# Performance work log

Measured on AMD Instinct MI355X. Metric: run time of the kernel, lower is better.

Reference implementation:

```python
import jax, jax.numpy as jnp
import numpy as np

B, DV, W, H = 64, 2048, 14, 14
DQ, DA, G, DH, NC = 2400, 1200, 2, 1200, 3000


def setup_inputs() -> dict:
    key = jax.random.key(0)
    ks = jax.random.split(key, 14)
    s = lambda k, shp, scale=0.02: jax.random.normal(k, shp, dtype=jnp.float32) * scale
    return {
        "input_q": jax.random.normal(ks[0], (B, DQ), dtype=jnp.float32),
        "input_v": jax.random.normal(ks[1], (B, DV, W, H), dtype=jnp.float32),
        "Wv_att": s(ks[2], (DA, DV)),
        "bv_att": s(ks[3], (DA,)),
        "Wq_att": s(ks[4], (DA, DQ)),
        "bq_att": s(ks[5], (DA,)),
        "Watt": s(ks[6], (G, DA)),
        "batt": s(ks[7], (G,)),
        "Wv_fus": s(ks[8], (G, DH, DV)),
        "bv_fus": s(ks[9], (G, DH)),
        "Wq_fus": s(ks[10], (G * DH, DQ)),
        "bq_fus": s(ks[11], (G * DH,)),
        "Wc": s(ks[12], (NC, G * DH)),
        "bc": s(ks[13], (NC,)),
    }


def reference(input_q, input_v, Wv_att, bv_att, Wq_att, bq_att, Watt, batt,
              Wv_fus, bv_fus, Wq_fus, bq_fus, Wc, bc):
    b, dv, w, h = input_v.shape
    n = w * h  # spatial positions

    # --- attention branch (eval mode: dropout = identity) ---
    # 1x1 conv == per-position linear over channels; activation_v = tanh
    xv = jnp.tanh(jnp.einsum('bchw,dc->bdhw', input_v, Wv_att) + bv_att[None, :, None, None])
    xv = xv.reshape(b, -1, n).transpose(0, 2, 1)               # [B, WH, DA]
    # question projection; activation_q = tanh
    xq = jnp.tanh(input_q @ Wq_att.T + bq_att)                 # [B, DA]
    # MLB Hadamard fusion + activation_mm = tanh
    xatt = jnp.tanh(xv * xq[:, None, :])                       # [B, WH, DA]
    # glimpse scores: 1x1 conv over dim_mm channels
    wgt = jnp.einsum('bnd,gd->bgn', xatt, Watt) + batt[None, :, None]  # [B, G, WH]
    att = jax.nn.softmax(wgt, axis=-1)                         # softmax over WH per glimpse

    # weighted sum of ORIGINAL features per glimpse
    v_flat = input_v.reshape(b, dv, n)                         # [B, DV, WH]
    v_att = jnp.einsum('bgn,bdn->bgd', att, v_flat)            # [B, G, DV]

    # --- glimpse fusion + classification ---
    v_fus = jnp.tanh(jnp.einsum('bgd,ghd->bgh', v_att, Wv_fus) + bv_fus)  # [B, G, DH]
    v_fus = v_fus.reshape(b, -1)                               # [B, G*DH] (concat over glimpses)
    q_fus = jnp.tanh(input_q @ Wq_fus.T + bq_fus)              # [B, G*DH]
    x = (v_fus * q_fus) @ Wc.T + bc                            # [B, NC]
    return (x, wgt)
```

## Files before the change

### kernel.cpp

```cpp
#include <hip/hip_runtime.h>
#include <hip/hip_fp16.h>

typedef _Float16 half8 __attribute__((ext_vector_type(8)));
typedef float f32x4 __attribute__((ext_vector_type(4)));

__device__ __forceinline__ float tanh_fast(float x) {
  float e = __expf(2.0f * x);
  return 1.0f - 2.0f / (e + 1.0f);
}

__device__ __forceinline__ void gload16(const _Float16* g, _Float16* l) {
  __builtin_amdgcn_global_load_lds((const __attribute__((address_space(1))) void*)g,
                                   (__attribute__((address_space(3))) void*)l,
                                   16, 0, 0);
}

__global__ __launch_bounds__(256) void k_transpose_v(const float* __restrict__ in,
                                                     _Float16* __restrict__ out) {
  __shared__ float t[64][65];
  int b = blockIdx.z;
  int c0 = blockIdx.y * 64;
  int p0 = blockIdx.x * 64;
  int tid = threadIdx.x;
  int pl = tid & 63;
  #pragma unroll
  for (int s = 0; s < 16; ++s) {
    int cl = (tid >> 6) + s * 4;
    int p = p0 + pl;
    t[cl][pl] = (p < 196) ? in[((size_t)b * 2048 + (c0 + cl)) * 196 + p] : 0.0f;
  }
  __syncthreads();
  int c8 = (tid & 7) * 8;
  #pragma unroll
  for (int s = 0; s < 2; ++s) {
    int p = p0 + (tid >> 3) + s * 32;
    if (p < 196) {
      half8 v;
      #pragma unroll
      for (int j = 0; j < 8; ++j) v[j] = (_Float16)t[c8 + j][(tid >> 3) + s * 32];
      *(half8*)(out + ((size_t)b * 196 + p) * 2048 + c0 + c8) = v;
    }
  }
}

__global__ __launch_bounds__(256) void k_prep(const float* __restrict__ W,
                                              _Float16* __restrict__ Wh,
                                              const float* __restrict__ batt,
                                              float* __restrict__ wgt) {
  int i = blockIdx.x * 256 + threadIdx.x;
  int n = i >> 11;
  Wh[i] = (n < 1200) ? (_Float16)W[i] : (_Float16)0.0f;
  if (i < 25088) wgt[i] = batt[(i / 196) & 1];
}

__global__ __launch_bounds__(256) void k_gemm1(const _Float16* __restrict__ A,
                                               const _Float16* __restrict__ B,
                                               const float* __restrict__ bias,
                                               const float* __restrict__ xq,
                                               const float* __restrict__ Watt,
                                               float* __restrict__ wgt) {
  __shared__ __align__(16) _Float16 As[128 * 64];
  __shared__ __align__(16) _Float16 Bs[128 * 64];
  int tid = threadIdx.x;
  int n0 = blockIdx.x * 128;
  int m0 = blockIdx.y * 128;
  int lane = tid & 63;
  int wave = tid >> 6;
  int wm = (wave >> 1) * 64;
  int wn = (wave & 1) * 64;
  int fr = lane & 15;
  int fq = lane >> 4;

  int rsub = lane >> 3;
  int gchunk = (lane & 7) ^ rsub;
  const _Float16* aSrc = A + (size_t)(m0 + wave * 8 + rsub) * 2048 + gchunk * 8;
  const _Float16* bSrc = B + (size_t)(n0 + wave * 8 + rsub) * 2048 + gchunk * 8;
  _Float16* aDst = As + (wave * 8) * 64;
  _Float16* bDst = Bs + (wave * 8) * 64;

  f32x4 acc[4][4];
  #pragma unroll
  for (int i = 0; i < 4; ++i)
    #pragma unroll
    for (int j = 0; j < 4; ++j) acc[i][j] = (f32x4){0.f, 0.f, 0.f, 0.f};

  for (int kt = 0; kt < 32; ++kt) {
    int k0 = kt * 64;
    __syncthreads();
    #pragma unroll
    for (int j = 0; j < 4; ++j) {
      gload16(aSrc + k0 + (size_t)j * 32 * 2048, aDst + j * 32 * 64);
      gload16(bSrc + k0 + (size_t)j * 32 * 2048, bDst + j * 32 * 64);
    }
    __syncthreads();
    #pragma unroll
    for (int s = 0; s < 2; ++s) {
      half8 af[4], bf[4];
      #pragma unroll
      for (int mt = 0; mt < 4; ++mt) {
        int row = wm + mt * 16 + fr;
        af[mt] = *(const half8*)(As + row * 64 + (((s * 4 + fq) ^ (fr & 7)) << 3));
      }
      #pragma unroll
      for (int nt = 0; nt < 4; ++nt) {
        int row = wn + nt * 16 + fr;
        bf[nt] = *(const half8*)(Bs + row * 64 + (((s * 4 + fq) ^ (fr & 7)) << 3));
      }
      #pragma unroll
      for (int mt = 0; mt < 4; ++mt)
        #pragma unroll
        for (int nt = 0; nt < 4; ++nt)
          acc[mt][nt] = __builtin_amdgcn_mfma_f32_16x16x32_f16(af[mt], bf[nt], acc[mt][nt], 0, 0, 0);
    }
  }

  float s0[16], s1[16];
  #pragma unroll
  for (int i = 0; i < 16; ++i) { s0[i] = 0.f; s1[i] = 0.f; }

  #pragma unroll
  for (int nt = 0; nt < 4; ++nt) {
    int col = n0 + wn + nt * 16 + fr;
    bool ok = col < 1200;
    float bcol = ok ? bias[col] : 0.f;
    float wa0 = ok ? Watt[col] : 0.f;
    float wa1 = ok ? Watt[1200 + col] : 0.f;
    #pragma unroll
    for (int mt = 0; mt < 4; ++mt) {
      #pragma unroll
      for (int r = 0; r < 4; ++r) {
        int row = m0 + wm + mt * 16 + fq * 4 + r;
        int b = row / 196;
        float xqv = ok ? xq[b * 1200 + col] : 0.f;
        float xv = tanh_fast(acc[mt][nt][r] + bcol);
        float xa = tanh_fast(xv * xqv);
        s0[mt * 4 + r] += xa * wa0;
        s1[mt * 4 + r] += xa * wa1;
      }
    }
  }
  #pragma unroll
  for (int i = 0; i < 16; ++i) {
    #pragma unroll
    for (int off = 8; off > 0; off >>= 1) {
      s0[i] += __shfl_down(s0[i], off);
      s1[i] += __shfl_down(s1[i], off);
    }
  }
  if (fr == 0) {
    #pragma unroll
    for (int i = 0; i < 16; ++i) {
      int row = m0 + wm + (i >> 2) * 16 + fq * 4 + (i & 3);
      int b = row / 196;
      int p = row - b * 196;
      atomicAdd(&wgt[(b * 2 + 0) * 196 + p], s0[i]);
      atomicAdd(&wgt[(b * 2 + 1) * 196 + p], s1[i]);
    }
  }
}

__global__ __launch_bounds__(64) void k_softmax(const float* __restrict__ wgt,
                                                float* __restrict__ att) {
  int bg = blockIdx.x;
  int lane = threadIdx.x;
  const float* wr = wgt + (size_t)bg * 196;
  float v[4];
  #pragma unroll
  for (int i = 0; i < 4; ++i) {
    int n = lane + i * 64;
    v[i] = (n < 196) ? wr[n] : -1e30f;
  }
  float mx = fmaxf(fmaxf(v[0], v[1]), fmaxf(v[2], v[3]));
  #pragma unroll
  for (int off = 32; off > 0; off >>= 1) mx = fmaxf(mx, __shfl_xor(mx, off));
  float s = 0.f;
  #pragma unroll
  for (int i = 0; i < 4; ++i) {
    int n = lane + i * 64;
    float e = (n < 196) ? __expf(v[i] - mx) : 0.f;
    v[i] = e;
    s += e;
  }
  #pragma unroll
  for (int off = 32; off > 0; off >>= 1) s += __shfl_xor(s, off);
  float inv = 1.f / s;
  #pragma unroll
  for (int i = 0; i < 4; ++i) {
    int n = lane + i * 64;
    if (n < 196) att[(size_t)bg * 196 + n] = v[i] * inv;
  }
}

__global__ __launch_bounds__(256) void k_vatt(const _Float16* __restrict__ Vt,
                                              const float* __restrict__ att,
                                              float* __restrict__ v_att) {
  __shared__ float a0s[196], a1s[196];
  int b = blockIdx.y;
  int tid = threadIdx.x;
  if (tid < 196) {
    a0s[tid] = att[((size_t)b * 2 + 0) * 196 + tid];
    a1s[tid] = att[((size_t)b * 2 + 1) * 196 + tid];
  }
  __syncthreads();
  int d = blockIdx.x * 256 + tid;
  const _Float16* vp = Vt + (size_t)b * 196 * 2048 + d;
  float s0 = 0.f, s1 = 0.f;
  for (int n = 0; n < 196; ++n) {
    float v = (float)vp[(size_t)n * 2048];
    s0 += a0s[n] * v;
    s1 += a1s[n] * v;
  }
  v_att[((size_t)b * 2 + 0) * 2048 + d] = s0;
  v_att[((size_t)b * 2 + 1) * 2048 + d] = s1;
}

__global__ __launch_bounds__(256) void k_skinny(const float* __restrict__ A1,
                                                const float* __restrict__ A2,
                                                int lda, int strideAz,
                                                const float* __restrict__ W, long strideWz,
                                                int N, int K, int S,
                                                float* __restrict__ P, int ldp, int colOffZ) {
  __shared__ __align__(16) float As[32][64];
  __shared__ __align__(16) float Ws2[32][64];
  int tid = threadIdx.x;
  int z = blockIdx.z;
  int s = blockIdx.y;
  int nt0 = blockIdx.x * 64;
  int tiles = K >> 5;
  int t0 = (s * tiles) / S;
  int t1 = ((s + 1) * tiles) / S;
  int tx = tid & 15, ty = tid >> 4;
  int lm = tid >> 2;
  int lk = (tid & 3) * 8;
  const float* Ab = A1 + (size_t)z * strideAz + (size_t)lm * lda;
  const float* A2b = A2 ? (A2 + (size_t)z * strideAz + (size_t)lm * lda) : nullptr;
  int ng = nt0 + lm;
  const float* Wb = W + (size_t)z * strideWz + (size_t)ng * K;
  bool wok = ng < N;
  float acc[4][4] = {};
  for (int t = t0; t < t1; ++t) {
    int k0 = t * 32;
    __syncthreads();
    #pragma unroll
    for (int j = 0; j < 8; ++j) {
      float v = Ab[k0 + lk + j];
      if (A2b) v *= A2b[k0 + lk + j];
      As[lk + j][lm] = v;
    }
    #pragma unroll
    for (int j = 0; j < 8; ++j) Ws2[lk + j][lm] = wok ? Wb[k0 + lk + j] : 0.0f;
    __syncthreads();
    #pragma unroll
    for (int kk = 0; kk < 32; ++kk) {
      f32x4 a = *(const f32x4*)&As[kk][ty * 4];
      f32x4 wv = *(const f32x4*)&Ws2[kk][tx * 4];
      #pragma unroll
      for (int i = 0; i < 4; ++i)
        #pragma unroll
        for (int j = 0; j < 4; ++j) acc[i][j] += a[i] * wv[j];
    }
  }
  #pragma unroll
  for (int i = 0; i < 4; ++i) {
    int m = ty * 4 + i;
    #pragma unroll
    for (int j = 0; j < 4; ++j) {
      int nl = nt0 + tx * 4 + j;
      if (nl < N) P[((size_t)s * 64 + m) * ldp + z * colOffZ + nl] = acc[i][j];
    }
  }
}

__global__ __launch_bounds__(256) void k_combine(const float* __restrict__ P, int S, int ldp,
                                                 const float* __restrict__ bias,
                                                 float* __restrict__ out, int total, int act) {
  int i = blockIdx.x * 256 + threadIdx.x;
  if (i >= total) return;
  int col = i % ldp;
  float sum = bias[col];
  for (int ss = 0; ss < S; ++ss) sum += P[(size_t)ss * total + i];
  out[i] = act ? tanh_fast(sum) : sum;
}

extern "C" void kernel_launch(void* const* d_in, const int* in_sizes, int n_in,
                              void* d_out, int out_size, void* d_ws, size_t ws_size,
                              hipStream_t stream) {
  const float* input_q = (const float*)d_in[0];
  const float* input_v = (const float*)d_in[1];
  const float* Wv_att  = (const float*)d_in[2];
  const float* bv_att  = (const float*)d_in[3];
  const float* Wq_att  = (const float*)d_in[4];
  const float* bq_att  = (const float*)d_in[5];
  const float* Watt    = (const float*)d_in[6];
  const float* batt    = (const float*)d_in[7];
  const float* Wv_fus  = (const float*)d_in[8];
  const float* bv_fus  = (const float*)d_in[9];
  const float* Wq_fus  = (const float*)d_in[10];
  const float* bq_fus  = (const float*)d_in[11];
  const float* Wc      = (const float*)d_in[12];
  const float* bc      = (const float*)d_in[13];
  float* out = (float*)d_out;

  char* ws = (char*)d_ws;
  _Float16* Vt   = (_Float16*)ws; ws += 51380224;
  _Float16* Wh   = (_Float16*)ws; ws += 5242880;
  float* xq      = (float*)ws;    ws += 307200;
  float* att     = (float*)ws;    ws += 100352;
  float* v_att   = (float*)ws;    ws += 1048576;
  float* v_fus   = (float*)ws;    ws += 614400;
  float* q_fus   = (float*)ws;    ws += 614400;
  float* P       = (float*)ws;    ws += 14745600;

  float* x_out   = out;
  float* wgt_out = out + 192000;

  const int S = 16;

  k_transpose_v<<<dim3(4, 32, 64), dim3(256), 0, stream>>>(input_v, Vt);
  k_prep<<<dim3(10240), dim3(256), 0, stream>>>(Wv_att, Wh, batt, wgt_out);

  k_skinny<<<dim3(19, S, 1), dim3(256), 0, stream>>>(input_q, nullptr, 2400, 0,
                                                     Wq_att, 0, 1200, 2400, S, P, 1200, 0);
  k_combine<<<dim3(300), dim3(256), 0, stream>>>(P, S, 1200, bq_att, xq, 76800, 1);

  k_skinny<<<dim3(38, S, 1), dim3(256), 0, stream>>>(input_q, nullptr, 2400, 0,
                                                     Wq_fus, 0, 2400, 2400, S, P + 1228800, 2400, 0);
  k_combine<<<dim3(600), dim3(256), 0, stream>>>(P + 1228800, S, 2400, bq_fus, q_fus, 153600, 1);

  k_gemm1<<<dim3(10, 98), dim3(256), 0, stream>>>(Vt, Wh, bv_att, xq, Watt, wgt_out);

  k_softmax<<<dim3(128), dim3(64), 0, stream>>>(wgt_out, att);

  k_vatt<<<dim3(8, 64), dim3(256), 0, stream>>>(Vt, att, v_att);

  k_skinny<<<dim3(19, S, 2), dim3(256), 0, stream>>>(v_att, nullptr, 4096, 2048,
                                                     Wv_fus, 1200L * 2048L, 1200, 2048, S, P, 2400, 1200);
  k_combine<<<dim3(600), dim3(256), 0, stream>>>(P, S, 2400, bv_fus, v_fus, 153600, 1);

  k_skinny<<<dim3(47, S, 1), dim3(256), 0, stream>>>(v_fus, q_fus, 2400, 0,
                                                     Wc, 0, 3000, 2400, S, P, 3000, 0);
  k_combine<<<dim3(750), dim3(256), 0, stream>>>(P, S, 3000, bc, x_out, 192000, 0);
}
```

Baseline: 514.7 us.

## Fuse launches: merged prep kernel, atomic split-K, softmax into vatt, deferred tanh

```diff
diff --git a/kernel.cpp b/kernel.cpp
--- a/kernel.cpp
+++ b/kernel.cpp
@@ -15,42 +15,57 @@
                                    16, 0, 0);
 }
 
-__global__ __launch_bounds__(256) void k_transpose_v(const float* __restrict__ in,
-                                                     _Float16* __restrict__ out) {
-  __shared__ float t[64][65];
-  int b = blockIdx.z;
-  int c0 = blockIdx.y * 64;
-  int p0 = blockIdx.x * 64;
-  int tid = threadIdx.x;
-  int pl = tid & 63;
-  #pragma unroll
-  for (int s = 0; s < 16; ++s) {
-    int cl = (tid >> 6) + s * 4;
-    int p = p0 + pl;
-    t[cl][pl] = (p < 196) ? in[((size_t)b * 2048 + (c0 + cl)) * 196 + p] : 0.0f;
-  }
-  __syncthreads();
-  int c8 = (tid & 7) * 8;
-  #pragma unroll
-  for (int s = 0; s < 2; ++s) {
-    int p = p0 + (tid >> 3) + s * 32;
-    if (p < 196) {
-      half8 v;
-      #pragma unroll
-      for (int j = 0; j < 8; ++j) v[j] = (_Float16)t[c8 + j][(tid >> 3) + s * 32];
-      *(half8*)(out + ((size_t)b * 196 + p) * 2048 + c0 + c8) = v;
-    }
-  }
-}
-
-__global__ __launch_bounds__(256) void k_prep(const float* __restrict__ W,
+__global__ __launch_bounds__(256) void k_misc(const float* __restrict__ in_v,
+                                              _Float16* __restrict__ Vt,
+                                              const float* __restrict__ Wv,
                                               _Float16* __restrict__ Wh,
                                               const float* __restrict__ batt,
-                                              float* __restrict__ wgt) {
-  int i = blockIdx.x * 256 + threadIdx.x;
-  int n = i >> 11;
-  Wh[i] = (n < 1200) ? (_Float16)W[i] : (_Float16)0.0f;
-  if (i < 25088) wgt[i] = batt[(i / 196) & 1];
+                                              const float* __restrict__ bq_att,
+                                              const float* __restrict__ bq_fus,
+                                              const float* __restrict__ bv_fus,
+                                              const float* __restrict__ bc,
+                                              float* __restrict__ wgt,
+                                              float* __restrict__ xq,
+                                              float* __restrict__ qfus,
+                                              float* __restrict__ vfus,
+                                              float* __restrict__ xout) {
+  int blk = blockIdx.x;
+  int tid = threadIdx.x;
+  if (blk < 8192) {
+    __shared__ float t[64][65];
+    int x = blk & 3, y = (blk >> 2) & 31, b = blk >> 7;
+    int c0 = y * 64, p0 = x * 64;
+    int pl = tid & 63;
+    #pragma unroll
+    for (int s = 0; s < 16; ++s) {
+      int cl = (tid >> 6) + s * 4;
+      int p = p0 + pl;
+      t[cl][pl] = (p < 196) ? in_v[((size_t)b * 2048 + (c0 + cl)) * 196 + p] : 0.0f;
+    }
+    __syncthreads();
+    int c8 = (tid & 7) * 8;
+    #pragma unroll
+    for (int s = 0; s < 2; ++s) {
+      int p = p0 + (tid >> 3) + s * 32;
+      if (p < 196) {
+        half8 v;
+        #pragma unroll
+        for (int j = 0; j < 8; ++j) v[j] = (_Float16)t[c8 + j][(tid >> 3) + s * 32];
+        *(half8*)(Vt + ((size_t)b * 196 + p) * 2048 + c0 + c8) = v;
+      }
+    }
+  } else {
+    int j = (blk - 8192) * 256 + tid;
+    int n = j >> 11;
+    Wh[j] = (n < 1200) ? (_Float16)Wv[j] : (_Float16)0.0f;
+    if (j < 601088) {
+      if (j < 25088)       wgt[j]  = batt[(j / 196) & 1];
+      else if (j < 101888) { int i = j - 25088;  xq[i]   = bq_att[i % 1200]; }
+      else if (j < 255488) { int i = j - 101888; qfus[i] = bq_fus[i % 2400]; }
+      else if (j < 409088) { int i = j - 255488; vfus[i] = bv_fus[i % 2400]; }
+      else                 { int i = j - 409088; xout[i] = bc[i % 3000]; }
+    }
+  }
 }
 
 __global__ __launch_bounds__(256) void k_gemm1(const _Float16* __restrict__ A,
@@ -131,7 +146,7 @@
       for (int r = 0; r < 4; ++r) {
         int row = m0 + wm + mt * 16 + fq * 4 + r;
         int b = row / 196;
-        float xqv = ok ? xq[b * 1200 + col] : 0.f;
+        float xqv = ok ? tanh_fast(xq[b * 1200 + col]) : 0.f;
         float xv = tanh_fast(acc[mt][nt][r] + bcol);
         float xa = tanh_fast(xv * xqv);
         s0[mt * 4 + r] += xa * wa0;
@@ -159,47 +174,41 @@
   }
 }
 
-__global__ __launch_bounds__(64) void k_softmax(const float* __restrict__ wgt,
-                                                float* __restrict__ att) {
-  int bg = blockIdx.x;
-  int lane = threadIdx.x;
-  const float* wr = wgt + (size_t)bg * 196;
-  float v[4];
-  #pragma unroll
-  for (int i = 0; i < 4; ++i) {
-    int n = lane + i * 64;
-    v[i] = (n < 196) ? wr[n] : -1e30f;
-  }
-  float mx = fmaxf(fmaxf(v[0], v[1]), fmaxf(v[2], v[3]));
-  #pragma unroll
-  for (int off = 32; off > 0; off >>= 1) mx = fmaxf(mx, __shfl_xor(mx, off));
-  float s = 0.f;
-  #pragma unroll
-  for (int i = 0; i < 4; ++i) {
-    int n = lane + i * 64;
-    float e = (n < 196) ? __expf(v[i] - mx) : 0.f;
-    v[i] = e;
-    s += e;
-  }
-  #pragma unroll
-  for (int off = 32; off > 0; off >>= 1) s += __shfl_xor(s, off);
-  float inv = 1.f / s;
-  #pragma unroll
-  for (int i = 0; i < 4; ++i) {
-    int n = lane + i * 64;
-    if (n < 196) att[(size_t)bg * 196 + n] = v[i] * inv;
-  }
-}
-
 __global__ __launch_bounds__(256) void k_vatt(const _Float16* __restrict__ Vt,
-                                              const float* __restrict__ att,
+                                              const float* __restrict__ wgt,
                                               float* __restrict__ v_att) {
   __shared__ float a0s[196], a1s[196];
   int b = blockIdx.y;
   int tid = threadIdx.x;
-  if (tid < 196) {
-    a0s[tid] = att[((size_t)b * 2 + 0) * 196 + tid];
-    a1s[tid] = att[((size_t)b * 2 + 1) * 196 + tid];
+  int wv = tid >> 6, lane = tid & 63;
+  if (wv < 2) {
+    const float* wr = wgt + ((size_t)b * 2 + wv) * 196;
+    float v[4];
+    #pragma unroll
+    for (int i = 0; i < 4; ++i) {
+      int n = lane + i * 64;
+      v[i] = (n < 196) ? wr[n] : -1e30f;
+    }
+    float mx = fmaxf(fmaxf(v[0], v[1]), fmaxf(v[2], v[3]));
+    #pragma unroll
+    for (int off = 32; off > 0; off >>= 1) mx = fmaxf(mx, __shfl_xor(mx, off));
+    float s = 0.f;
+    #pragma unroll
+    for (int i = 0; i < 4; ++i) {
+      int n = lane + i * 64;
+      float e = (n < 196) ? __expf(v[i] - mx) : 0.f;
+      v[i] = e;
+      s += e;
+    }
+    #pragma unroll
+    for (int off = 32; off > 0; off >>= 1) s += __shfl_xor(s, off);
+    float inv = 1.f / s;
+    float* dst = wv ? a1s : a0s;
+    #pragma unroll
+    for (int i = 0; i < 4; ++i) {
+      int n = lane + i * 64;
+      if (n < 196) dst[n] = v[i] * inv;
+    }
   }
   __syncthreads();
   int d = blockIdx.x * 256 + tid;
@@ -214,12 +223,72 @@
   v_att[((size_t)b * 2 + 1) * 2048 + d] = s1;
 }
 
+__global__ __launch_bounds__(256) void k_skinnyQ(const float* __restrict__ q,
+                                                 const float* __restrict__ Wa,
+                                                 const float* __restrict__ Wf,
+                                                 int S,
+                                                 float* __restrict__ xq,
+                                                 float* __restrict__ qfus) {
+  __shared__ __align__(16) float As[32][64];
+  __shared__ __align__(16) float Ws2[32][64];
+  int tid = threadIdx.x;
+  int x = blockIdx.x;
+  int s = blockIdx.y;
+  bool f = x >= 19;
+  const float* W = f ? Wf : Wa;
+  int nt0 = f ? (x - 19) * 64 : x * 64;
+  int N = f ? 2400 : 1200;
+  const int K = 2400;
+  int tiles = K >> 5;
+  int t0 = (s * tiles) / S;
+  int t1 = ((s + 1) * tiles) / S;
+  int tx = tid & 15, ty = tid >> 4;
+  int lm = tid >> 2;
+  int lk = (tid & 3) * 8;
+  const float* Ab = q + (size_t)lm * K;
+  int ng = nt0 + lm;
+  const float* Wb = W + (size_t)ng * K;
+  bool wok = ng < N;
+  float acc[4][4] = {};
+  for (int t = t0; t < t1; ++t) {
+    int k0 = t * 32;
+    __syncthreads();
+    #pragma unroll
+    for (int j = 0; j < 8; ++j) As[lk + j][lm] = Ab[k0 + lk + j];
+    #pragma unroll
+    for (int j = 0; j < 8; ++j) Ws2[lk + j][lm] = wok ? Wb[k0 + lk + j] : 0.0f;
+    __syncthreads();
+    #pragma unroll
+    for (int kk = 0; kk < 32; ++kk) {
+      f32x4 a = *(const f32x4*)&As[kk][ty * 4];
+      f32x4 wv = *(const f32x4*)&Ws2[kk][tx * 4];
+      #pragma unroll
+      for (int i = 0; i < 4; ++i)
+        #pragma unroll
+        for (int j = 0; j < 4; ++j) acc[i][j] += a[i] * wv[j];
+    }
+  }
+  #pragma unroll
+  for (int i = 0; i < 4; ++i) {
+    int m = ty * 4 + i;
+    #pragma unroll
+    for (int j = 0; j < 4; ++j) {
+      int nl = nt0 + tx * 4 + j;
+      if (nl < N) {
+        if (f) atomicAdd(&qfus[m * 2400 + nl], acc[i][j]);
+        else   atomicAdd(&xq[m * 1200 + nl], acc[i][j]);
+      }
+    }
+  }
+}
+
 __global__ __launch_bounds__(256) void k_skinny(const float* __restrict__ A1,
                                                 const float* __restrict__ A2,
                                                 int lda, int strideAz,
                                                 const float* __restrict__ W, long strideWz,
                                                 int N, int K, int S,
-                                                float* __restrict__ P, int ldp, int colOffZ) {
+                                                float* __restrict__ Out, int ldOut,
+                                                int colOffZ, int mode) {
   __shared__ __align__(16) float As[32][64];
   __shared__ __align__(16) float Ws2[32][64];
   int tid = threadIdx.x;
@@ -244,7 +313,7 @@
     #pragma unroll
     for (int j = 0; j < 8; ++j) {
       float v = Ab[k0 + lk + j];
-      if (A2b) v *= A2b[k0 + lk + j];
+      if (mode) v = tanh_fast(v) * tanh_fast(A2b[k0 + lk + j]);
       As[lk + j][lm] = v;
     }
     #pragma unroll
@@ -266,20 +335,9 @@
     #pragma unroll
     for (int j = 0; j < 4; ++j) {
       int nl = nt0 + tx * 4 + j;
-      if (nl < N) P[((size_t)s * 64 + m) * ldp + z * colOffZ + nl] = acc[i][j];
-    }
-  }
-}
-
-__global__ __launch_bounds__(256) void k_combine(const float* __restrict__ P, int S, int ldp,
-                                                 const float* __restrict__ bias,
-                                                 float* __restrict__ out, int total, int act) {
-  int i = blockIdx.x * 256 + threadIdx.x;
-  if (i >= total) return;
-  int col = i % ldp;
-  float sum = bias[col];
-  for (int ss = 0; ss < S; ++ss) sum += P[(size_t)ss * total + i];
-  out[i] = act ? tanh_fast(sum) : sum;
+      if (nl < N) atomicAdd(&Out[(size_t)m * ldOut + z * colOffZ + nl], acc[i][j]);
+    }
+  }
 }
 
 extern "C" void kernel_launch(void* const* d_in, const int* in_sizes, int n_in,
@@ -305,39 +363,30 @@
   _Float16* Vt   = (_Float16*)ws; ws += 51380224;
   _Float16* Wh   = (_Float16*)ws; ws += 5242880;
   float* xq      = (float*)ws;    ws += 307200;
-  float* att     = (float*)ws;    ws += 100352;
   float* v_att   = (float*)ws;    ws += 1048576;
   float* v_fus   = (float*)ws;    ws += 614400;
   float* q_fus   = (float*)ws;    ws += 614400;
-  float* P       = (float*)ws;    ws += 14745600;
 
   float* x_out   = out;
   float* wgt_out = out + 192000;
 
-  const int S = 16;
-
-  k_transpose_v<<<dim3(4, 32, 64), dim3(256), 0, stream>>>(input_v, Vt);
-  k_prep<<<dim3(10240), dim3(256), 0, stream>>>(Wv_att, Wh, batt, wgt_out);
-
-  k_skinny<<<dim3(19, S, 1), dim3(256), 0, stream>>>(input_q, nullptr, 2400, 0,
-                                                     Wq_att, 0, 1200, 2400, S, P, 1200, 0);
-  k_combine<<<dim3(300), dim3(256), 0, stream>>>(P, S, 1200, bq_att, xq, 76800, 1);
-
-  k_skinny<<<dim3(38, S, 1), dim3(256), 0, stream>>>(input_q, nullptr, 2400, 0,
-                                                     Wq_fus, 0, 2400, 2400, S, P + 1228800, 2400, 0);
-  k_combine<<<dim3(600), dim3(256), 0, stream>>>(P + 1228800, S, 2400, bq_fus, q_fus, 153600, 1);
+  const int S = 8;
+
+  k_misc<<<dim3(18432), dim3(256), 0, stream>>>(input_v, Vt, Wv_att, Wh,
+                                                batt, bq_att, bq_fus, bv_fus, bc,
+                                                wgt_out, xq, q_fus, v_fus, x_out);
+
+  k_skinnyQ<<<dim3(57, S), dim3(256), 0, stream>>>(input_q, Wq_att, Wq_fus, S, xq, q_fus);
 
   k_gemm1<<<dim3(10, 98), dim3(256), 0, stream>>>(Vt, Wh, bv_att, xq, Watt, wgt_out);
 
-  k_softmax<<<dim3(128), dim3(64), 0, stream>>>(wgt_out, att);
-
-  k_vatt<<<dim3(8, 64), dim3(256), 0, stream>>>(Vt, att, v_att);
+  k_vatt<<<dim3(8, 64), dim3(256), 0, stream>>>(Vt, wgt_out, v_att);
 
   k_skinny<<<dim3(19, S, 2), dim3(256), 0, stream>>>(v_att, nullptr, 4096, 2048,
-                                                     Wv_fus, 1200L * 2048L, 1200, 2048, S, P, 2400, 1200);
-  k_combine<<<dim3(600), dim3(256), 0, stream>>>(P, S, 2400, bv_fus, v_fus, 153600, 1);
+                                                     Wv_fus, 1200L * 2048L, 1200, 2048, S,
+                                                     v_fus, 2400, 1200, 0);
 
   k_skinny<<<dim3(47, S, 1), dim3(256), 0, stream>>>(v_fus, q_fus, 2400, 0,
-                                                     Wc, 0, 3000, 2400, S, P, 3000, 0);
-  k_combine<<<dim3(750), dim3(256), 0, stream>>>(P, S, 3000, bc, x_out, 192000, 0);
-}
+                                                     Wc, 0, 3000, 2400, S,
+                                                     x_out, 3000, 0, 1);
+}
```

Result: slower. 531.7 us (+3.3%).
